# Performance work log

Measured on AMD Instinct MI355X. Metric: run time of the kernel, lower is better.

## Reference

```python
import jax, jax.numpy as jnp
import numpy as np

HEAD_SIZE = 64

def setup_inputs() -> dict:
    key = jax.random.key(0)
    k1, k2, k3, k4 = jax.random.split(key, 4)
    B, T, C = 4, 4096, 1024
    x = jax.random.normal(k1, (B, T, C), dtype=jnp.float32)
    scale = 1.0 / np.sqrt(C)
    Wk = jax.random.normal(k2, (C, HEAD_SIZE), dtype=jnp.float32) * scale
    Wq = jax.random.normal(k3, (C, HEAD_SIZE), dtype=jnp.float32) * scale
    Wv = jax.random.normal(k4, (C, HEAD_SIZE), dtype=jnp.float32) * scale
    return {"x": x, "Wk": Wk, "Wq": Wq, "Wv": Wv}

def reference(x, Wk, Wq, Wv):
    B, T, C = x.shape
    k = jnp.einsum('btc,ch->bth', x, Wk)   # [B,T,H]
    q = jnp.einsum('btc,ch->bth', x, Wq)
    v = jnp.einsum('btc,ch->bth', x, Wv)
    # Faithful to the source: scores = k @ q^T (NOT the usual q @ k^T)
    wei = jnp.einsum('bth,bsh->bts', k, q) * (HEAD_SIZE ** -0.5)  # [B,T,T]
    causal = jnp.tril(jnp.ones((T, T), dtype=bool))
    wei = jnp.where(causal, wei, -jnp.inf)
    wei = jax.nn.softmax(wei, axis=-1)
    # dropout_rate = 0.0 -> identity
    out = jnp.einsum('bts,bsh->bth', wei, v)  # [B,T,H]
    return out
```

## Files before the change

### kernel.cpp

```cpp
#include <hip/hip_runtime.h>


typedef __attribute__((ext_vector_type(8))) short short8;
typedef __attribute__((ext_vector_type(4))) short s16x4;
typedef __attribute__((ext_vector_type(4))) float f32x4;
typedef unsigned short u16;

#define MFMA16(A, B, C) __builtin_amdgcn_mfma_f32_16x16x32_bf16((A), (B), (C), 0, 0, 0)

__device__ __forceinline__ u16 f2b(float f) {
    __bf16 h = (__bf16)f;
    return __builtin_bit_cast(u16, h);
}
__device__ __forceinline__ float b2f(u16 v) {
    return __builtin_bit_cast(float, (unsigned int)v << 16);
}

__device__ __forceinline__ void gload16(const void* g, void* l) {
    __builtin_amdgcn_global_load_lds(
        (const __attribute__((address_space(1))) unsigned int*)g,
        (__attribute__((address_space(3))) unsigned int*)l, 16, 0, 0);
}

__global__ __launch_bounds__(256) void wt_kernel(const float* __restrict__ Wk,
                                                 const float* __restrict__ Wq,
                                                 const float* __restrict__ Wv,
                                                 u16* __restrict__ WtF) {
    const int kc = blockIdx.x;
    const int mat = blockIdx.y;
    const float* W = (mat == 0) ? Wk : (mat == 1 ? Wq : Wv);
    const int tid = threadIdx.x;
    const int tl = tid >> 6, lane = tid & 63, quad = lane >> 4, l16 = lane & 15;
    short8 v;
#pragma unroll
    for (int j = 0; j < 8; ++j)
        v[j] = f2b(W[(size_t)(kc * 32 + quad * 8 + j) * 64 + tl * 16 + l16]);
    const size_t dst = ((size_t)((mat * 4 + tl) * 32 + kc) * 64 + lane) * 8;
#pragma unroll
    for (int rep = 0; rep < 8; ++rep)
        *(short8*)(WtF + (size_t)rep * 196608 + dst) = v;
}

__global__ __launch_bounds__(256) void proj_kernel(const float* __restrict__ x,
                                                   const u16* __restrict__ WtF,
                                                   u16* __restrict__ Kb,
                                                   u16* __restrict__ Qb,
                                                   u16* __restrict__ Vt) {
    __shared__ char smem[65536];
    const int tid = threadIdx.x;
    const int w = tid >> 6, lane = tid & 63, quad = lane >> 4, l16 = lane & 15;
    const int mbase = blockIdx.x * 32;
    const u16* Wrep = WtF + (size_t)(blockIdx.x & 7) * 196608;
    const char* xblk = (const char*)x + (size_t)mbase * 4096;
    const int wbase16 = (w << 6) * 16;

    f32x4 acc[2][3];
#pragma unroll
    for (int r = 0; r < 2; ++r)
#pragma unroll
        for (int c = 0; c < 3; ++c) acc[r][c] = (f32x4)(0.0f);

#define STAGE(buf, p) do {                                                          \
        char* la = smem + (buf) * 8192;                                             \
        char* lb = smem + 16384 + (buf) * 24576;                                    \
        _Pragma("unroll")                                                           \
        for (int i = 0; i < 2; ++i) {                                               \
            int u = i * 256 + tid;                                                  \
            int row = u >> 4;                                                       \
            int cb = ((u & 15) * 16) ^ ((row & 7) << 5);                            \
            gload16(xblk + (size_t)row * 4096 + (size_t)(p) * 256 + cb,             \
                    la + i * 4096 + wbase16);                                       \
        }                                                                           \
        _Pragma("unroll")                                                           \
        for (int i = 0; i < 6; ++i) {                                               \
            int u = i * 256 + tid;                                                  \
            gload16(Wrep + (size_t)(u >> 7) * 16384 + (size_t)(p) * 1024 + (u & 127) * 8, \
                    lb + i * 4096 + wbase16);                                       \
        }                                                                           \
    } while (0)

    STAGE(0, 0);
    __syncthreads();

    for (int t = 0; t < 16; ++t) {
        const int cur = t & 1;
        if (t < 15) STAGE(cur ^ 1, t + 1);
        const char* Ab = smem + cur * 8192;
        const char* Bb = smem + 16384 + cur * 24576;
#pragma unroll
        for (int kk = 0; kk < 2; ++kk) {
            short8 af[2];
#pragma unroll
            for (int r = 0; r < 2; ++r) {
                const int row = r * 16 + l16;
                const int c0 = (kk * 128 + quad * 32) ^ ((l16 & 7) << 5);
                f32x4 lo = *(const f32x4*)(Ab + row * 256 + c0);
                f32x4 hi = *(const f32x4*)(Ab + row * 256 + (c0 ^ 16));
                short8 a;
#pragma unroll
                for (int j = 0; j < 4; ++j) {
                    a[j]     = (short)f2b(lo[j]);
                    a[j + 4] = (short)f2b(hi[j]);
                }
                af[r] = a;
            }
#pragma unroll
            for (int c = 0; c < 3; ++c) {
                short8 bf = *(const short8*)(Bb + (((w * 3 + c) * 2 + kk) * 64 + lane) * 16);
                acc[0][c] = MFMA16(af[0], bf, acc[0][c]);
                acc[1][c] = MFMA16(af[1], bf, acc[1][c]);
            }
        }
        __syncthreads();
    }
#undef STAGE

    u16 (*tile)[200] = (u16(*)[200])smem;
#pragma unroll
    for (int r = 0; r < 2; ++r)
#pragma unroll
        for (int c = 0; c < 3; ++c)
#pragma unroll
            for (int reg = 0; reg < 4; ++reg)
                tile[r * 16 + quad * 4 + reg][(w * 3 + c) * 16 + l16] = f2b(acc[r][c][reg]);
    __syncthreads();

    const int b = mbase >> 12, t0b = mbase & 4095;
    {
        const int row = tid >> 3, cu8 = (tid & 7) * 8;
        short8 vk = *(const short8*)&tile[row][cu8];
        *(short8*)(Kb + (size_t)(mbase + row) * 64 + cu8) = vk;
        short8 vq = *(const short8*)&tile[row][64 + cu8];
#pragma unroll
        for (int r = 0; r < 4; ++r)
            *(short8*)(Qb + (size_t)r * 1048576 + (size_t)(mbase + row) * 64 + cu8) = vq;
    }
    {
        const int h = tid >> 2, toff = (tid & 3) * 8;
        short8 vv;
#pragma unroll
        for (int j = 0; j < 8; ++j) vv[j] = tile[toff + j][128 + h];
#pragma unroll
        for (int r = 0; r < 4; ++r)
            *(short8*)(Vt + (size_t)r * 1048576 + ((size_t)(b * 64 + h) << 12) + t0b + toff) = vv;
    }
}

#define QSWZ(row, cb) ((row) * 128 + ((cb) ^ (((row) & 7) << 4)))
__global__ __launch_bounds__(256) void attn_kernel(const u16* __restrict__ Kb,
                                                   const u16* __restrict__ Qb,
                                                   const u16* __restrict__ Vt,
                                                   u16* __restrict__ Op,
                                                   float* __restrict__ Ml) {
    const int pc = blockIdx.x;
    const int b = blockIdx.y;
    const int pair = pc / 9, c9 = pc - pair * 9;
    const int nLow = (pair >> 3) + 1;
    const int tile  = (c9 < nLow) ? pair : (63 - pair);
    const int chunk = (c9 < nLow) ? c9 : (c9 - nLow);
    __shared__ u16 Qs[64 * 64];
    __shared__ u16 Vs[64 * 64];
    __shared__ u16 Ps[4][16][72];
    const int tid = threadIdx.x;
    const int w = tid >> 6, lane = tid & 63, quad = lane >> 4, l16 = lane & 15;
    const int t0 = tile * 64;
    const int stBeg = chunk * 8;
    const int stEnd = min(chunk * 8 + 7, tile);

    const u16* Qp = Qb + (size_t)(tile & 3) * 1048576;
    const u16* Vp = Vt + (size_t)(tile & 3) * 1048576;

    const int lin0 = tid, lin1 = tid + 256;
    const int qd0 = QSWZ(lin0 >> 3, (lin0 & 7) * 16);
    const int qd1 = QSWZ(lin1 >> 3, (lin1 & 7) * 16);
    const size_t vrow0 = ((size_t)(b * 64 + (lin0 >> 3)) << 12) + (lin0 & 7) * 8;
    const size_t vrow1 = ((size_t)(b * 64 + (lin1 >> 3)) << 12) + (lin1 & 7) * 8;

    short8 aK[2];
#pragma unroll
    for (int kk = 0; kk < 2; ++kk)
        aK[kk] = *(const short8*)(Kb + (size_t)((b << 12) + t0 + w * 16 + l16) * 64 + kk * 32 + quad * 8);

    short8 qr0 = *(const short8*)(Qp + (size_t)((b << 12) + stBeg * 64) * 64 + lin0 * 8);
    short8 qr1 = *(const short8*)(Qp + (size_t)((b << 12) + stBeg * 64) * 64 + lin1 * 8);
    short8 vr0 = *(const short8*)(Vp + vrow0 + stBeg * 64);
    short8 vr1 = *(const short8*)(Vp + vrow1 + stBeg * 64);

    float l_acc[4] = {0.0f, 0.0f, 0.0f, 0.0f};
    f32x4 O[4];
#pragma unroll
    for (int nt = 0; nt < 4; ++nt) O[nt] = (f32x4)(0.0f);

    const int trow = w * 16 + quad * 4;
    const int tglob = t0 + trow;

    for (int st = stBeg; st <= stEnd; ++st) {
        const int s0 = st * 64;
        __syncthreads();
        *(short8*)((char*)Qs + qd0) = qr0;
        *(short8*)((char*)Qs + qd1) = qr1;
        *(short8*)((char*)Vs + qd0) = vr0;
        *(short8*)((char*)Vs + qd1) = vr1;
        __syncthreads();
        if (st < stEnd) {
            qr0 = *(const short8*)(Qp + (size_t)((b << 12) + (st + 1) * 64) * 64 + lin0 * 8);
            qr1 = *(const short8*)(Qp + (size_t)((b << 12) + (st + 1) * 64) * 64 + lin1 * 8);
            vr0 = *(const short8*)(Vp + vrow0 + (st + 1) * 64);
            vr1 = *(const short8*)(Vp + vrow1 + (st + 1) * 64);
        }

        f32x4 sc[4];
#pragma unroll
        for (int nt = 0; nt < 4; ++nt) sc[nt] = (f32x4)(0.0f);
#pragma unroll
        for (int kk = 0; kk < 2; ++kk)
#pragma unroll
            for (int nt = 0; nt < 4; ++nt) {
                short8 bq = *(const short8*)((const char*)Qs + QSWZ(nt * 16 + l16, kk * 64 + quad * 16));
                sc[nt] = MFMA16(aK[kk], bq, sc[nt]);
            }

#pragma unroll
        for (int nt = 0; nt < 4; ++nt) {
            int sg = s0 + nt * 16 + l16;
#pragma unroll
            for (int reg = 0; reg < 4; ++reg) {
                float v = sc[nt][reg];
                if (st == tile && sg > tglob + reg) v = -1e30f;
                float p = exp2f(v * 0.18033688011112042f);
                l_acc[reg] += p;
                Ps[w][quad * 4 + reg][nt * 16 + l16] = f2b(p);
            }
        }

#pragma unroll
        for (int kk = 0; kk < 2; ++kk) {
            short8 ap = *(const short8*)&Ps[w][l16][kk * 32 + quad * 8];
#pragma unroll
            for (int nt = 0; nt < 4; ++nt) {
                short8 bv = *(const short8*)((const char*)Vs + QSWZ(nt * 16 + l16, kk * 64 + quad * 16));
                O[nt] = MFMA16(ap, bv, O[nt]);
            }
        }
    }

    const int slot = ((b * 64 + tile) * 8 + chunk);
    {
#pragma unroll
        for (int reg = 0; reg < 4; ++reg) {
            float v = l_acc[reg];
            v += __shfl_xor(v, 1);
            v += __shfl_xor(v, 2);
            v += __shfl_xor(v, 4);
            v += __shfl_xor(v, 8);
            if (l16 == 0) Ml[(size_t)slot * 64 + trow + reg] = v;
        }
    }
#pragma unroll
    for (int nt = 0; nt < 4; ++nt)
#pragma unroll
        for (int reg = 0; reg < 4; ++reg)
            Op[(size_t)slot * 4096 + (size_t)(trow + reg) * 64 + nt * 16 + l16] = f2b(O[nt][reg]);
}

__global__ __launch_bounds__(256) void combine_kernel(const u16* __restrict__ Op,
                                                      const float* __restrict__ Ml,
                                                      float* __restrict__ out) {
    const int tid = threadIdx.x, cu = tid & 7, r0 = tid >> 3;
    const int tile = blockIdx.x, b = blockIdx.y;
    const int nch = tile / 8 + 1;
    const int slotBase = (b * 64 + tile) * 8;
#pragma unroll
    for (int i = 0; i < 2; ++i) {
        const int row = r0 + 32 * i;
        float L = 0.0f, acc[8];
#pragma unroll
        for (int j = 0; j < 8; ++j) acc[j] = 0.0f;
#pragma unroll
        for (int c = 0; c < 8; ++c) {
            const bool act = c < nch;
            float lraw = Ml[(size_t)(slotBase + c) * 64 + row];
            short8 ov = *(const short8*)(Op + (size_t)(slotBase + c) * 4096 + (size_t)row * 64 + cu * 8);
            L += act ? lraw : 0.0f;
#pragma unroll
            for (int j = 0; j < 8; ++j)
                acc[j] += act ? b2f((u16)ov[j]) : 0.0f;
        }
        float inv = 1.0f / L;
        float* dst = out + ((size_t)(b << 12) + tile * 64 + row) * 64 + cu * 8;
        *(float4*)(dst)     = make_float4(acc[0] * inv, acc[1] * inv, acc[2] * inv, acc[3] * inv);
        *(float4*)(dst + 4) = make_float4(acc[4] * inv, acc[5] * inv, acc[6] * inv, acc[7] * inv);
    }
}

extern "C" void kernel_launch(void* const* d_in, const int* in_sizes, int n_in,
                              void* d_out, int out_size, void* d_ws, size_t ws_size,
                              hipStream_t stream) {
    const float* x  = (const float*)d_in[0];
    const float* Wk = (const float*)d_in[1];
    const float* Wq = (const float*)d_in[2];
    const float* Wv = (const float*)d_in[3];

    u16* ws16 = (u16*)d_ws;
    u16* Wt = ws16;
    u16* Kb = Wt + 1572864;
    u16* Qb = Kb + 1048576;
    u16* Vt = Qb + 4194304;
    u16* Op = Vt + 4194304;
    float* Ml = (float*)(Op + 8388608);

    wt_kernel<<<dim3(32, 3), 256, 0, stream>>>(Wk, Wq, Wv, Wt);
    proj_kernel<<<512, 256, 0, stream>>>(x, Wt, Kb, Qb, Vt);
    attn_kernel<<<dim3(288, 4), 256, 0, stream>>>(Kb, Qb, Vt, Op, Ml);
    combine_kernel<<<dim3(64, 4), 256, 0, stream>>>(Op, Ml, (float*)d_out);
}
```

Baseline: 151.2 us.

## Process 128-wide key blocks per iteration with transposed score MFMA layout

The attention loop now handles 128 source positions per iteration instead of 64, so each chunk covers four blocks and there are half as many barrier and LDS staging rounds. The score MFMA operands are swapped so each lane holds four consecutive source columns, which lets P be written to LDS as packed 4-element vectors and turns the row-sum reduction into two cross-quad shuffles. The cost is more registers, a larger shared-memory footprint (about 49 KB), and more wasted work on the diagonal block, because masking now applies to a 128-wide tile.

```diff
diff --git a/kernel.cpp b/kernel.cpp
--- a/kernel.cpp
+++ b/kernel.cpp
@@ -147,6 +147,7 @@
 }
 
 #define QSWZ(row, cb) ((row) * 128 + ((cb) ^ (((row) & 7) << 4)))
+#define VSWZ(row, cb) ((row) * 256 + ((cb) ^ (((row) & 15) << 4)))
 __global__ __launch_bounds__(256) void attn_kernel(const u16* __restrict__ Kb,
                                                    const u16* __restrict__ Qb,
                                                    const u16* __restrict__ Vt,
@@ -158,109 +159,116 @@
     const int nLow = (pair >> 3) + 1;
     const int tile  = (c9 < nLow) ? pair : (63 - pair);
     const int chunk = (c9 < nLow) ? c9 : (c9 - nLow);
-    __shared__ u16 Qs[64 * 64];
-    __shared__ u16 Vs[64 * 64];
-    __shared__ u16 Ps[4][16][72];
+    __shared__ char smem[50176];
+    u16* Qs = (u16*)smem;
+    u16* Vs = (u16*)(smem + 16384);
     const int tid = threadIdx.x;
     const int w = tid >> 6, lane = tid & 63, quad = lane >> 4, l16 = lane & 15;
+    char* psB = smem + 32768 + w * 4352;
     const int t0 = tile * 64;
-    const int stBeg = chunk * 8;
-    const int stEnd = min(chunk * 8 + 7, tile);
+    const int bsBeg = chunk * 4;
+    const int bsEnd = min(chunk * 4 + 3, tile >> 1);
+    const int bsDiag = tile >> 1;
 
     const u16* Qp = Qb + (size_t)(tile & 3) * 1048576;
     const u16* Vp = Vt + (size_t)(tile & 3) * 1048576;
 
-    const int lin0 = tid, lin1 = tid + 256;
-    const int qd0 = QSWZ(lin0 >> 3, (lin0 & 7) * 16);
-    const int qd1 = QSWZ(lin1 >> 3, (lin1 & 7) * 16);
-    const size_t vrow0 = ((size_t)(b * 64 + (lin0 >> 3)) << 12) + (lin0 & 7) * 8;
-    const size_t vrow1 = ((size_t)(b * 64 + (lin1 >> 3)) << 12) + (lin1 & 7) * 8;
+    int qd[4], vd[4];
+    size_t qg[4], vg[4];
+#pragma unroll
+    for (int i = 0; i < 4; ++i) {
+        const int lin = tid + i * 256;
+        qd[i] = QSWZ(lin >> 3, (lin & 7) * 16);
+        vd[i] = VSWZ(lin >> 4, (lin & 15) * 16);
+        qg[i] = ((size_t)(b << 12) + (lin >> 3)) * 64 + (lin & 7) * 8;
+        vg[i] = ((size_t)(b * 64 + (lin >> 4)) << 12) + (lin & 15) * 8;
+    }
 
     short8 aK[2];
 #pragma unroll
     for (int kk = 0; kk < 2; ++kk)
         aK[kk] = *(const short8*)(Kb + (size_t)((b << 12) + t0 + w * 16 + l16) * 64 + kk * 32 + quad * 8);
 
-    short8 qr0 = *(const short8*)(Qp + (size_t)((b << 12) + stBeg * 64) * 64 + lin0 * 8);
-    short8 qr1 = *(const short8*)(Qp + (size_t)((b << 12) + stBeg * 64) * 64 + lin1 * 8);
-    short8 vr0 = *(const short8*)(Vp + vrow0 + stBeg * 64);
-    short8 vr1 = *(const short8*)(Vp + vrow1 + stBeg * 64);
-
-    float l_acc[4] = {0.0f, 0.0f, 0.0f, 0.0f};
+    short8 qr[4], vr[4];
+#pragma unroll
+    for (int i = 0; i < 4; ++i) {
+        qr[i] = *(const short8*)(Qp + qg[i] + (size_t)bsBeg * 8192);
+        vr[i] = *(const short8*)(Vp + vg[i] + bsBeg * 128);
+    }
+
+    float l_acc = 0.0f;
     f32x4 O[4];
 #pragma unroll
-    for (int nt = 0; nt < 4; ++nt) O[nt] = (f32x4)(0.0f);
-
-    const int trow = w * 16 + quad * 4;
-    const int tglob = t0 + trow;
-
-    for (int st = stBeg; st <= stEnd; ++st) {
-        const int s0 = st * 64;
+    for (int ht = 0; ht < 4; ++ht) O[ht] = (f32x4)(0.0f);
+
+    const int tg = t0 + w * 16 + l16;
+
+    for (int bs = bsBeg; bs <= bsEnd; ++bs) {
         __syncthreads();
-        *(short8*)((char*)Qs + qd0) = qr0;
-        *(short8*)((char*)Qs + qd1) = qr1;
-        *(short8*)((char*)Vs + qd0) = vr0;
-        *(short8*)((char*)Vs + qd1) = vr1;
+#pragma unroll
+        for (int i = 0; i < 4; ++i) {
+            *(short8*)(smem + qd[i]) = qr[i];
+            *(short8*)(smem + 16384 + vd[i]) = vr[i];
+        }
         __syncthreads();
-        if (st < stEnd) {
-            qr0 = *(const short8*)(Qp + (size_t)((b << 12) + (st + 1) * 64) * 64 + lin0 * 8);
-            qr1 = *(const short8*)(Qp + (size_t)((b << 12) + (st + 1) * 64) * 64 + lin1 * 8);
-            vr0 = *(const short8*)(Vp + vrow0 + (st + 1) * 64);
-            vr1 = *(const short8*)(Vp + vrow1 + (st + 1) * 64);
-        }
-
-        f32x4 sc[4];
-#pragma unroll
-        for (int nt = 0; nt < 4; ++nt) sc[nt] = (f32x4)(0.0f);
+        if (bs < bsEnd) {
+#pragma unroll
+            for (int i = 0; i < 4; ++i) {
+                qr[i] = *(const short8*)(Qp + qg[i] + (size_t)(bs + 1) * 8192);
+                vr[i] = *(const short8*)(Vp + vg[i] + (bs + 1) * 128);
+            }
+        }
+
+        f32x4 sc[8];
+#pragma unroll
+        for (int nt = 0; nt < 8; ++nt) sc[nt] = (f32x4)(0.0f);
 #pragma unroll
         for (int kk = 0; kk < 2; ++kk)
 #pragma unroll
-            for (int nt = 0; nt < 4; ++nt) {
-                short8 bq = *(const short8*)((const char*)Qs + QSWZ(nt * 16 + l16, kk * 64 + quad * 16));
-                sc[nt] = MFMA16(aK[kk], bq, sc[nt]);
-            }
-
-#pragma unroll
-        for (int nt = 0; nt < 4; ++nt) {
-            int sg = s0 + nt * 16 + l16;
+            for (int nt = 0; nt < 8; ++nt) {
+                short8 aq = *(const short8*)(smem + QSWZ(nt * 16 + l16, kk * 64 + quad * 16));
+                sc[nt] = MFMA16(aq, aK[kk], sc[nt]);
+            }
+
+#pragma unroll
+        for (int nt = 0; nt < 8; ++nt) {
+            const int sgBase = bs * 128 + nt * 16 + quad * 4;
+            s16x4 v4;
 #pragma unroll
             for (int reg = 0; reg < 4; ++reg) {
                 float v = sc[nt][reg];
-                if (st == tile && sg > tglob + reg) v = -1e30f;
+                if (bs == bsDiag && sgBase + reg > tg) v = -1e30f;
                 float p = exp2f(v * 0.18033688011112042f);
-                l_acc[reg] += p;
-                Ps[w][quad * 4 + reg][nt * 16 + l16] = f2b(p);
-            }
-        }
-
-#pragma unroll
-        for (int kk = 0; kk < 2; ++kk) {
-            short8 ap = *(const short8*)&Ps[w][l16][kk * 32 + quad * 8];
-#pragma unroll
-            for (int nt = 0; nt < 4; ++nt) {
-                short8 bv = *(const short8*)((const char*)Vs + QSWZ(nt * 16 + l16, kk * 64 + quad * 16));
-                O[nt] = MFMA16(ap, bv, O[nt]);
+                l_acc += p;
+                v4[reg] = (short)f2b(p);
+            }
+            *(s16x4*)(psB + l16 * 272 + nt * 32 + quad * 8) = v4;
+        }
+
+#pragma unroll
+        for (int kk = 0; kk < 4; ++kk) {
+            short8 ap = *(const short8*)(psB + l16 * 272 + kk * 64 + quad * 16);
+#pragma unroll
+            for (int ht = 0; ht < 4; ++ht) {
+                short8 bv = *(const short8*)(smem + 16384 + VSWZ(ht * 16 + l16, kk * 64 + quad * 16));
+                O[ht] = MFMA16(ap, bv, O[ht]);
             }
         }
     }
 
     const int slot = ((b * 64 + tile) * 8 + chunk);
     {
-#pragma unroll
-        for (int reg = 0; reg < 4; ++reg) {
-            float v = l_acc[reg];
-            v += __shfl_xor(v, 1);
-            v += __shfl_xor(v, 2);
-            v += __shfl_xor(v, 4);
-            v += __shfl_xor(v, 8);
-            if (l16 == 0) Ml[(size_t)slot * 64 + trow + reg] = v;
-        }
-    }
-#pragma unroll
-    for (int nt = 0; nt < 4; ++nt)
+        float v = l_acc;
+        v += __shfl_xor(v, 16);
+        v += __shfl_xor(v, 32);
+        if (quad == 0) Ml[(size_t)slot * 64 + w * 16 + l16] = v;
+    }
+    const int trow = w * 16 + quad * 4;
+#pragma unroll
+    for (int ht = 0; ht < 4; ++ht)
 #pragma unroll
         for (int reg = 0; reg < 4; ++reg)
-            Op[(size_t)slot * 4096 + (size_t)(trow + reg) * 64 + nt * 16 + l16] = f2b(O[nt][reg]);
+            Op[(size_t)slot * 4096 + (size_t)(trow + reg) * 64 + ht * 16 + l16] = f2b(O[ht][reg]);
 }
 
 __global__ __launch_bounds__(256) void combine_kernel(const u16* __restrict__ Op,
```

Measured after the change: 149.0 us. No clear change (-1.5%).
